# Performance work log

Hardware: AMD Instinct MI355X
Metric: run time of the kernel (lower is better)

## Reference

```python
import jax, jax.numpy as jnp
import numpy as np

B, T, E, H, V = 64, 512, 512, 512, 50000

def setup_inputs() -> dict:
    key = jax.random.key(0)
    ks = jax.random.split(key, 8)
    x = jax.random.randint(ks[0], (B, T), 0, V)
    h0 = jax.random.normal(ks[1], (B, H), jnp.float32) * 0.1
    c0 = jax.random.normal(ks[2], (B, H), jnp.float32) * 0.1
    emb = jax.random.normal(ks[3], (V, E), jnp.float32) * 0.02
    emb = emb.at[0].set(0.0)  # padding_idx=0
    s_i = 1.0 / np.sqrt(H)
    W_ih = jax.random.uniform(ks[4], (4 * H, E), jnp.float32, -s_i, s_i)
    W_hh = jax.random.uniform(ks[5], (4 * H, H), jnp.float32, -s_i, s_i)
    b_ih = jax.random.uniform(ks[6], (4 * H,), jnp.float32, -s_i, s_i)
    b_hh = jax.random.uniform(ks[7], (4 * H,), jnp.float32, -s_i, s_i)
    return {"x": x, "h0": h0, "c0": c0, "emb": emb,
            "W_ih": W_ih, "W_hh": W_hh, "b_ih": b_ih, "b_hh": b_hh}

def reference(x, h0, c0, emb, W_ih, W_hh, b_ih, b_hh):
    # embedding lookup (option 'a'): [B, T, E]
    xs = emb[x]
    # precompute input-to-gate projections for all timesteps: [B, T, 4H]
    pre = jnp.einsum('bte,ge->btg', xs, W_ih) + b_ih + b_hh
    pre_t = jnp.swapaxes(pre, 0, 1)  # [T, B, 4H]

    def step(carry, p_t):
        h, c = carry
        gates = p_t + h @ W_hh.T  # [B, 4H]
        i, f, g, o = jnp.split(gates, 4, axis=-1)
        i = jax.nn.sigmoid(i)
        f = jax.nn.sigmoid(f)
        g = jnp.tanh(g)
        o = jax.nn.sigmoid(o)
        c_new = f * c + i * g
        h_new = o * jnp.tanh(c_new)
        return (h_new, c_new), h_new

    _, hs = jax.lax.scan(step, (h0, c0), pre_t)  # hs: [T, B, H]
    # original stacks per-batch lists of per-timestep hidden states -> [B, T, H]
    return jnp.swapaxes(hs, 0, 1)
```

## Files before the change

kernel.cpp:

```cpp
#include <hip/hip_runtime.h>
#include <stdint.h>

typedef __attribute__((ext_vector_type(8))) short short8;
typedef __attribute__((ext_vector_type(4))) float f4;
typedef __attribute__((ext_vector_type(4))) uint32_t u32x4;

#define B_ 64
#define T_ 512
#define E_ 512
#define H_ 512
#define GH 2048

static __device__ __forceinline__ uint16_t f2bf(float f) {
  uint32_t u = __builtin_bit_cast(uint32_t, f);
  uint32_t r = (u + 0x7FFFu + ((u >> 16) & 1u)) >> 16;
  return (uint16_t)r;
}
static __device__ __forceinline__ float bf2f(uint16_t b) {
  return __builtin_bit_cast(float, (uint32_t)b << 16);
}
static __device__ __forceinline__ float sigmoidf_(float x) {
  return 1.0f / (1.0f + __expf(-x));
}
static __device__ __forceinline__ float tanhf_(float x) {
  float e = __expf(-2.0f * fabsf(x));
  float t = (1.0f - e) / (1.0f + e);
  return __builtin_copysignf(t, x);
}

static __device__ __forceinline__ int ld_flag_cc(const int* p) {
  int v;
  asm volatile("global_load_dword %0, %1, off sc0 sc1\n\ts_waitcnt vmcnt(0)"
               : "=v"(v) : "v"(p) : "memory");
  return v;
}
static __device__ __forceinline__ void ld_x4_cc(u32x4* d, const void* p) {
  asm volatile("global_load_dwordx4 %0, %1, off sc0 sc1" : "=v"(*d) : "v"(p));
}
static __device__ __forceinline__ void st_u16_cc(uint16_t* p, uint32_t v) {
  asm volatile("global_store_short %0, %1, off sc0 sc1" :: "v"(p), "v"(v) : "memory");
}
static __device__ __forceinline__ void st_flag_cc(int* p, int v) {
  asm volatile("global_store_dword %0, %1, off sc0 sc1" :: "v"(p), "v"(v) : "memory");
}

__global__ void k_prep(const float* __restrict__ Whh, uint16_t* __restrict__ Whi_g,
                       uint16_t* __restrict__ Wlo_g) {
  int i = blockIdx.x * 256 + threadIdx.x;
  float w = Whh[i];
  uint16_t hi = f2bf(w);
  Whi_g[i] = hi;
  Wlo_g[i] = f2bf(w - bf2f(hi));
}

__global__ void k_init(const float* __restrict__ h0, uint16_t* __restrict__ hHi0,
                       uint16_t* __restrict__ hLo0, int* __restrict__ flags) {
  int i = blockIdx.x * 256 + threadIdx.x;
  if (i < B_ * H_) {
    float v = h0[i];
    uint16_t hi = f2bf(v);
    hHi0[i] = hi;
    hLo0[i] = f2bf(v - bf2f(hi));
  }
  if (i < 128) flags[i] = 0;
}

__launch_bounds__(256)
__global__ void k_pre(const int* __restrict__ x, const float* __restrict__ emb,
                      const float* __restrict__ Wih, const float* __restrict__ bih,
                      const float* __restrict__ bhh, float* __restrict__ pre2, int t0) {
  __shared__ uint16_t As[128 * 64];
  __shared__ uint16_t Bs[128 * 64];
  const int tid = threadIdx.x;
  const int tm = blockIdx.x >> 4;
  const int tn = blockIdx.x & 15;
  const int wid = tid >> 6, lane = tid & 63;
  const int wr = wid >> 1, wc = wid & 1;

  const int arow = tid >> 1;
  const int half = tid & 1;
  const int m = tm * 128 + arow;
  const int bb = m & 63;
  const int tt = t0 + (m >> 6);
  const int xid = x[bb * T_ + tt];
  const float* asrc = emb + (size_t)xid * E_ + half * 32;
  const float* bsrc = Wih + (size_t)(tn * 128 + arow) * E_ + half * 32;

  f4 acc[4][4];
#pragma unroll
  for (int a = 0; a < 4; ++a)
#pragma unroll
    for (int b = 0; b < 4; ++b) acc[a][b] = (f4){0.f, 0.f, 0.f, 0.f};

  for (int kk = 0; kk < 8; ++kk) {
    __syncthreads();
#pragma unroll
    for (int gi = 0; gi < 4; ++gi) {
      f4 a0 = *(const f4*)(asrc + kk * 64 + gi * 8);
      f4 a1 = *(const f4*)(asrc + kk * 64 + gi * 8 + 4);
      f4 b0 = *(const f4*)(bsrc + kk * 64 + gi * 8);
      f4 b1 = *(const f4*)(bsrc + kk * 64 + gi * 8 + 4);
      short8 va, vb;
#pragma unroll
      for (int j = 0; j < 4; ++j) {
        va[j] = (short)f2bf(a0[j]); va[4 + j] = (short)f2bf(a1[j]);
        vb[j] = (short)f2bf(b0[j]); vb[4 + j] = (short)f2bf(b1[j]);
      }
      int kq = half * 4 + gi;
      *(short8*)(As + arow * 64 + (kq ^ (arow & 7)) * 8) = va;
      *(short8*)(Bs + arow * 64 + (kq ^ (arow & 7)) * 8) = vb;
    }
    __syncthreads();
#pragma unroll
    for (int ks = 0; ks < 2; ++ks) {
      short8 af[4], bfr[4];
#pragma unroll
      for (int mi = 0; mi < 4; ++mi) {
        int row = wr * 64 + mi * 16 + (lane & 15);
        int kq = ks * 4 + (lane >> 4);
        af[mi] = *(const short8*)(As + row * 64 + (kq ^ (row & 7)) * 8);
      }
#pragma unroll
      for (int ni = 0; ni < 4; ++ni) {
        int row = wc * 64 + ni * 16 + (lane & 15);
        int kq = ks * 4 + (lane >> 4);
        bfr[ni] = *(const short8*)(Bs + row * 64 + (kq ^ (row & 7)) * 8);
      }
#pragma unroll
      for (int mi = 0; mi < 4; ++mi)
#pragma unroll
        for (int ni = 0; ni < 4; ++ni)
          acc[mi][ni] = __builtin_amdgcn_mfma_f32_16x16x32_bf16(af[mi], bfr[ni], acc[mi][ni], 0, 0, 0);
    }
  }
#pragma unroll
  for (int ni = 0; ni < 4; ++ni) {
    int n = tn * 128 + wc * 64 + ni * 16 + (lane & 15);
    float bias = bih[n] + bhh[n];
    int q = n >> 9, u = n & 511;
    int ug = u >> 4, uloc = u & 15;
    int gl = q * 16 + uloc;
#pragma unroll
    for (int mi = 0; mi < 4; ++mi) {
      int mrow = tm * 128 + wr * 64 + mi * 16 + (lane >> 4) * 4;
      int trel = mrow >> 6;
      int bbr = mrow & 63;
      f4 vst;
#pragma unroll
      for (int j = 0; j < 4; ++j) vst[j] = acc[mi][ni][j] + bias;
      float* dst = pre2 + (((size_t)trel * 32 + ug) * 4 + (bbr >> 4)) * 1024 + gl * 16 + (bbr & 15);
      *(f4*)dst = vst;
    }
  }
}

__launch_bounds__(256)
__global__ void k_lstm(const float* __restrict__ pre2, const uint16_t* __restrict__ Whi_g,
                       const uint16_t* __restrict__ Wlo_g, const float* __restrict__ c0,
                       float* __restrict__ out, uint16_t* __restrict__ hHi0,
                       uint16_t* __restrict__ hHi1, uint16_t* __restrict__ hLo0,
                       uint16_t* __restrict__ hLo1, float* __restrict__ c_state,
                       int* __restrict__ flags, int t0, int TB) {
  extern __shared__ char smem[];
  uint16_t* WhiL = (uint16_t*)smem;
  uint16_t* WloL = (uint16_t*)(smem + 65536);
  uint16_t* Hh   = (uint16_t*)(smem + 131072);
  uint16_t* Hl   = (uint16_t*)(smem + 147456);

  const int tid = threadIdx.x;
  const int bg = blockIdx.x & 3;
  const int ug = blockIdx.x >> 2;
  const int wv = tid >> 6, lane = tid & 63;
  const int wi = lane & 15, hi4 = lane >> 4;
  const int q = wi & 3, v = wi >> 2;
  const int u = ug * 16 + wv * 4 + v;
  const int gl = q * 16 + wv * 4 + v;

  for (int it = 0; it < 16; ++it) {
    int gg = it * 256 + tid;
    int r = gg >> 6, kq = gg & 63;
    int grow = (r & 3) * 512 + ug * 16 + (r >> 4) * 4 + ((r >> 2) & 3);
    short8 whi = *(const short8*)(Whi_g + (size_t)grow * 512 + kq * 8);
    short8 wlo = *(const short8*)(Wlo_g + (size_t)grow * 512 + kq * 8);
    int kqs = (kq & ~7) | ((kq & 7) ^ (r & 7));
    *(short8*)(WhiL + r * 512 + kqs * 8) = whi;
    *(short8*)(WloL + r * 512 + kqs * 8) = wlo;
  }

  f4 c_reg;
  {
    const float* csrc = (t0 == 0) ? c0 : c_state;
    const int brow = bg * 16 + hi4 * 4;
#pragma unroll
    for (int j = 0; j < 4; ++j) c_reg[j] = csrc[(size_t)(brow + j) * H_ + u];
  }
  int* myflag = flags + bg * 32 + ug;
  __syncthreads();

  for (int s = t0 + 1; s <= t0 + TB; ++s) {
    const uint16_t* hsHi = (((s - 1) & 1) ? hHi1 : hHi0) + (size_t)bg * 16 * 512;
    const uint16_t* hsLo = (((s - 1) & 1) ? hLo1 : hLo0) + (size_t)bg * 16 * 512;
    uint16_t* hdHi = ((s & 1) ? hHi1 : hHi0) + (size_t)bg * 16 * 512;
    uint16_t* hdLo = ((s & 1) ? hLo1 : hLo0) + (size_t)bg * 16 * 512;

    f4 accA, accB, accC;
    {
      const float* pblk = pre2 + (((size_t)(s - 1 - t0) * 32 + ug) * 4 + bg) * 1024;
      accA = *(const f4*)(pblk + gl * 16 + hi4 * 4);
      accB = (f4){0.f, 0.f, 0.f, 0.f};
      accC = accB;
    }

    if (lane < 32) {
      const int* fp = flags + bg * 32 + lane;
      const int target = s - 1;
      int guard = 0;
      while (ld_flag_cc(fp) < target) {
        __builtin_amdgcn_s_sleep(1);
        if (++guard > (1 << 20)) break;
      }
    }

    u32x4 dh[4], dl[4];
#pragma unroll
    for (int jj = 0; jj < 4; ++jj) ld_x4_cc(&dh[jj], hsHi + (size_t)(jj * 256 + tid) * 8);
#pragma unroll
    for (int jj = 0; jj < 4; ++jj) ld_x4_cc(&dl[jj], hsLo + (size_t)(jj * 256 + tid) * 8);
    asm volatile("s_waitcnt vmcnt(0)" ::: "memory");
    __builtin_amdgcn_sched_barrier(0);
#pragma unroll
    for (int jj = 0; jj < 4; ++jj) { asm volatile("" : "+v"(dh[jj])); asm volatile("" : "+v"(dl[jj])); }
#pragma unroll
    for (int jj = 0; jj < 4; ++jj) {
      int gidx = jj * 256 + tid;
      int row = gidx >> 6, kq = gidx & 63;
      int kqs = (kq & ~7) | ((kq & 7) ^ (row & 7));
      *(u32x4*)(Hh + row * 512 + kqs * 8) = dh[jj];
      *(u32x4*)(Hl + row * 512 + kqs * 8) = dl[jj];
    }
    __syncthreads();

    const int br = wv * 16 + wi;
#pragma unroll 4
    for (int ks = 0; ks < 16; ++ks) {
      int kq = ks * 4 + hi4;
      int kqsA = (kq & ~7) | ((kq & 7) ^ (wi & 7));
      int kqsB = (kq & ~7) | ((kq & 7) ^ (br & 7));
      short8 ah = *(const short8*)(Hh + wi * 512 + kqsA * 8);
      short8 al = *(const short8*)(Hl + wi * 512 + kqsA * 8);
      short8 bh = *(const short8*)(WhiL + br * 512 + kqsB * 8);
      short8 bl = *(const short8*)(WloL + br * 512 + kqsB * 8);
      accA = __builtin_amdgcn_mfma_f32_16x16x32_bf16(ah, bh, accA, 0, 0, 0);
      accB = __builtin_amdgcn_mfma_f32_16x16x32_bf16(al, bh, accB, 0, 0, 0);
      accC = __builtin_amdgcn_mfma_f32_16x16x32_bf16(ah, bl, accC, 0, 0, 0);
    }

    const bool qb0 = (q & 1) != 0, qb1 = (q & 2) != 0;
    const int b = bg * 16 + hi4 * 4 + q;
    f4 a0;
#pragma unroll
    for (int j = 0; j < 4; ++j) a0[j] = accA[j] + accB[j] + accC[j];
    f4 x1, s1a, s1b, x2a, x2b;
#pragma unroll
    for (int j = 0; j < 4; ++j) x1[j] = __shfl_xor(a0[j], 1);
#pragma unroll
    for (int j = 0; j < 4; ++j) {
      s1a[j] = qb0 ? x1[j] : a0[j];
      s1b[j] = qb0 ? a0[j] : x1[j];
    }
#pragma unroll
    for (int j = 0; j < 4; ++j) {
      x2a[j] = __shfl_xor(s1a[j], 2);
      x2b[j] = __shfl_xor(s1b[j], 2);
    }
    f4 cn, hn;
#pragma unroll
    for (int j = 0; j < 4; ++j) {
      float gi = qb1 ? x2a[j] : s1a[j];
      float gg = qb1 ? s1a[j] : x2a[j];
      float gf = qb1 ? x2b[j] : s1b[j];
      float go = qb1 ? s1b[j] : x2b[j];
      float iv = sigmoidf_(gi);
      float fv = sigmoidf_(gf);
      float gv = tanhf_(gg);
      float ov = sigmoidf_(go);
      float c2 = fv * c_reg[j] + iv * gv;
      cn[j] = c2;
      hn[j] = ov * tanhf_(c2);
    }
    c_reg = cn;
    float s01 = qb0 ? hn[1] : hn[0];
    float s23 = qb0 ? hn[3] : hn[2];
    float hq = qb1 ? s23 : s01;

    uint16_t hhi = f2bf(hq);
    uint16_t hlo = f2bf(hq - bf2f(hhi));
    const int rowloc = hi4 * 4 + q;
    st_u16_cc(hdHi + (size_t)rowloc * 512 + u, (uint32_t)hhi);
    st_u16_cc(hdLo + (size_t)rowloc * 512 + u, (uint32_t)hlo);
    asm volatile("s_waitcnt vmcnt(0)" ::: "memory");
    __syncthreads();
    if (tid == 0) st_flag_cc(myflag, s);
    __builtin_nontemporal_store(hq, &out[(size_t)b * (T_ * H_) + (size_t)(s - 1) * H_ + u]);
  }

  {
    const bool qb0 = (q & 1) != 0, qb1 = (q & 2) != 0;
    const int b = bg * 16 + hi4 * 4 + q;
    float c01 = qb0 ? c_reg[1] : c_reg[0];
    float c23 = qb0 ? c_reg[3] : c_reg[2];
    c_state[(size_t)b * H_ + u] = qb1 ? c23 : c01;
  }
}

extern "C" void kernel_launch(void* const* d_in, const int* in_sizes, int n_in,
                              void* d_out, int out_size, void* d_ws, size_t ws_size,
                              hipStream_t stream) {
  (void)in_sizes; (void)n_in; (void)out_size;
  const int* x = (const int*)d_in[0];
  const float* h0 = (const float*)d_in[1];
  const float* c0 = (const float*)d_in[2];
  const float* emb = (const float*)d_in[3];
  const float* Wih = (const float*)d_in[4];
  const float* Whh = (const float*)d_in[5];
  const float* bih = (const float*)d_in[6];
  const float* bhh = (const float*)d_in[7];
  float* out = (float*)d_out;
  char* ws = (char*)d_ws;

  int* flags = (int*)ws;
  float* c_state = (float*)(ws + 4096);
  uint16_t* hHi0 = (uint16_t*)(ws + 135168);
  uint16_t* hHi1 = (uint16_t*)(ws + 135168 + 65536);
  uint16_t* hLo0 = (uint16_t*)(ws + 135168 + 2 * 65536);
  uint16_t* hLo1 = (uint16_t*)(ws + 135168 + 3 * 65536);
  uint16_t* Whi_g = (uint16_t*)(ws + 397312);
  uint16_t* Wlo_g = (uint16_t*)(ws + 2494464);
  float* pre2 = (float*)(ws + 4591616);

  int TB = 512;
  while (TB > 2 && (size_t)4591616 + (size_t)TB * 524288 > ws_size) TB >>= 1;

  (void)hipFuncSetAttribute(reinterpret_cast<const void*>(k_lstm),
                            hipFuncAttributeMaxDynamicSharedMemorySize, 163840);

  k_prep<<<dim3(4096), dim3(256), 0, stream>>>(Whh, Whi_g, Wlo_g);
  k_init<<<dim3(128), dim3(256), 0, stream>>>(h0, hHi0, hLo0, flags);
  for (int t0 = 0; t0 < 512; t0 += TB) {
    k_pre<<<dim3((TB * 64 / 128) * 16), dim3(256), 0, stream>>>(x, emb, Wih, bih, bhh, pre2, t0);
    k_lstm<<<dim3(128), dim3(256), 163840, stream>>>(pre2, Whi_g, Wlo_g, c0, out, hHi0, hHi1,
                                                     hLo0, hLo1, c_state, flags, t0, TB);
  }
}
```

Baseline: 2.484 ms.

## Pack hi/lo hidden state into one word and use per-wave flags

The bf16 hi and lo halves of each hidden value are now packed into a single 32-bit word, so the exchange between recurrent steps needs one store and one load stream instead of two. Readiness flags become per-wave (four per block), so each wave polls only the producers of its own 128-column slice and signals right after its own store, which removes the block-wide barrier before the flag store. A barrier after the MFMA loop protects the shared hidden-state buffers, and the sleep in the spin loop is dropped. The trade-off is more flag traffic and polling, plus unpacking work when writing shared memory.

```diff
diff --git a/kernel.cpp b/kernel.cpp
--- a/kernel.cpp
+++ b/kernel.cpp
@@ -2,6 +2,7 @@
 #include <stdint.h>
 
 typedef __attribute__((ext_vector_type(8))) short short8;
+typedef __attribute__((ext_vector_type(4))) short short4_;
 typedef __attribute__((ext_vector_type(4))) float f4;
 typedef __attribute__((ext_vector_type(4))) uint32_t u32x4;
 
@@ -37,8 +38,8 @@
 static __device__ __forceinline__ void ld_x4_cc(u32x4* d, const void* p) {
   asm volatile("global_load_dwordx4 %0, %1, off sc0 sc1" : "=v"(*d) : "v"(p));
 }
-static __device__ __forceinline__ void st_u16_cc(uint16_t* p, uint32_t v) {
-  asm volatile("global_store_short %0, %1, off sc0 sc1" :: "v"(p), "v"(v) : "memory");
+static __device__ __forceinline__ void st_u32_cc(uint32_t* p, uint32_t v) {
+  asm volatile("global_store_dword %0, %1, off sc0 sc1" :: "v"(p), "v"(v) : "memory");
 }
 static __device__ __forceinline__ void st_flag_cc(int* p, int v) {
   asm volatile("global_store_dword %0, %1, off sc0 sc1" :: "v"(p), "v"(v) : "memory");
@@ -53,16 +54,16 @@
   Wlo_g[i] = f2bf(w - bf2f(hi));
 }
 
-__global__ void k_init(const float* __restrict__ h0, uint16_t* __restrict__ hHi0,
-                       uint16_t* __restrict__ hLo0, int* __restrict__ flags) {
+__global__ void k_init(const float* __restrict__ h0, uint32_t* __restrict__ hP0,
+                       int* __restrict__ flags) {
   int i = blockIdx.x * 256 + threadIdx.x;
   if (i < B_ * H_) {
     float v = h0[i];
     uint16_t hi = f2bf(v);
-    hHi0[i] = hi;
-    hLo0[i] = f2bf(v - bf2f(hi));
-  }
-  if (i < 128) flags[i] = 0;
+    uint16_t lo = f2bf(v - bf2f(hi));
+    hP0[i] = (uint32_t)hi | ((uint32_t)lo << 16);
+  }
+  if (i < 512) flags[i] = 0;
 }
 
 __launch_bounds__(256)
@@ -157,9 +158,8 @@
 __launch_bounds__(256)
 __global__ void k_lstm(const float* __restrict__ pre2, const uint16_t* __restrict__ Whi_g,
                        const uint16_t* __restrict__ Wlo_g, const float* __restrict__ c0,
-                       float* __restrict__ out, uint16_t* __restrict__ hHi0,
-                       uint16_t* __restrict__ hHi1, uint16_t* __restrict__ hLo0,
-                       uint16_t* __restrict__ hLo1, float* __restrict__ c_state,
+                       float* __restrict__ out, uint32_t* __restrict__ hP0,
+                       uint32_t* __restrict__ hP1, float* __restrict__ c_state,
                        int* __restrict__ flags, int t0, int TB) {
   extern __shared__ char smem[];
   uint16_t* WhiL = (uint16_t*)smem;
@@ -194,14 +194,13 @@
 #pragma unroll
     for (int j = 0; j < 4; ++j) c_reg[j] = csrc[(size_t)(brow + j) * H_ + u];
   }
-  int* myflag = flags + bg * 32 + ug;
+  int* fl = flags + bg * 128;
+  int* myflag = fl + ug * 4 + wv;
   __syncthreads();
 
   for (int s = t0 + 1; s <= t0 + TB; ++s) {
-    const uint16_t* hsHi = (((s - 1) & 1) ? hHi1 : hHi0) + (size_t)bg * 16 * 512;
-    const uint16_t* hsLo = (((s - 1) & 1) ? hLo1 : hLo0) + (size_t)bg * 16 * 512;
-    uint16_t* hdHi = ((s & 1) ? hHi1 : hHi0) + (size_t)bg * 16 * 512;
-    uint16_t* hdLo = ((s & 1) ? hLo1 : hLo0) + (size_t)bg * 16 * 512;
+    const uint32_t* hsrc = (((s - 1) & 1) ? hP1 : hP0) + (size_t)bg * 16 * 512;
+    uint32_t* hdst = (s & 1) ? hP1 : hP0;
 
     f4 accA, accB, accC;
     {
@@ -212,31 +211,41 @@
     }
 
     if (lane < 32) {
-      const int* fp = flags + bg * 32 + lane;
+      const int* fp = fl + wv * 32 + lane;
       const int target = s - 1;
       int guard = 0;
       while (ld_flag_cc(fp) < target) {
-        __builtin_amdgcn_s_sleep(1);
-        if (++guard > (1 << 20)) break;
-      }
-    }
-
-    u32x4 dh[4], dl[4];
-#pragma unroll
-    for (int jj = 0; jj < 4; ++jj) ld_x4_cc(&dh[jj], hsHi + (size_t)(jj * 256 + tid) * 8);
-#pragma unroll
-    for (int jj = 0; jj < 4; ++jj) ld_x4_cc(&dl[jj], hsLo + (size_t)(jj * 256 + tid) * 8);
+        if (++guard > (1 << 16)) break;
+      }
+    }
+
+    u32x4 d[8];
+#pragma unroll
+    for (int jj = 0; jj < 8; ++jj) {
+      int local = jj * 64 + lane;
+      int row = local >> 5;
+      int u0v = wv * 128 + (local & 31) * 4;
+      ld_x4_cc(&d[jj], hsrc + (size_t)row * 512 + u0v);
+    }
     asm volatile("s_waitcnt vmcnt(0)" ::: "memory");
     __builtin_amdgcn_sched_barrier(0);
 #pragma unroll
-    for (int jj = 0; jj < 4; ++jj) { asm volatile("" : "+v"(dh[jj])); asm volatile("" : "+v"(dl[jj])); }
-#pragma unroll
-    for (int jj = 0; jj < 4; ++jj) {
-      int gidx = jj * 256 + tid;
-      int row = gidx >> 6, kq = gidx & 63;
+    for (int jj = 0; jj < 8; ++jj) asm volatile("" : "+v"(d[jj]));
+#pragma unroll
+    for (int jj = 0; jj < 8; ++jj) {
+      int local = jj * 64 + lane;
+      int row = local >> 5;
+      int u0v = wv * 128 + (local & 31) * 4;
+      int kq = u0v >> 3, half = (u0v >> 2) & 1;
       int kqs = (kq & ~7) | ((kq & 7) ^ (row & 7));
-      *(u32x4*)(Hh + row * 512 + kqs * 8) = dh[jj];
-      *(u32x4*)(Hl + row * 512 + kqs * 8) = dl[jj];
+      short4_ hh, hl;
+#pragma unroll
+      for (int i = 0; i < 4; ++i) {
+        hh[i] = (short)(d[jj][i] & 0xFFFFu);
+        hl[i] = (short)(d[jj][i] >> 16);
+      }
+      *(short4_*)(Hh + row * 512 + kqs * 8 + half * 4) = hh;
+      *(short4_*)(Hl + row * 512 + kqs * 8 + half * 4) = hl;
     }
     __syncthreads();
 
@@ -254,9 +263,11 @@
       accB = __builtin_amdgcn_mfma_f32_16x16x32_bf16(al, bh, accB, 0, 0, 0);
       accC = __builtin_amdgcn_mfma_f32_16x16x32_bf16(ah, bl, accC, 0, 0, 0);
     }
+    __syncthreads();
 
     const bool qb0 = (q & 1) != 0, qb1 = (q & 2) != 0;
-    const int b = bg * 16 + hi4 * 4 + q;
+    const int rowloc = hi4 * 4 + q;
+    const int b = bg * 16 + rowloc;
     f4 a0;
 #pragma unroll
     for (int j = 0; j < 4; ++j) a0[j] = accA[j] + accB[j] + accC[j];
@@ -295,12 +306,9 @@
 
     uint16_t hhi = f2bf(hq);
     uint16_t hlo = f2bf(hq - bf2f(hhi));
-    const int rowloc = hi4 * 4 + q;
-    st_u16_cc(hdHi + (size_t)rowloc * 512 + u, (uint32_t)hhi);
-    st_u16_cc(hdLo + (size_t)rowloc * 512 + u, (uint32_t)hlo);
+    st_u32_cc(hdst + (size_t)b * 512 + u, (uint32_t)hhi | ((uint32_t)hlo << 16));
     asm volatile("s_waitcnt vmcnt(0)" ::: "memory");
-    __syncthreads();
-    if (tid == 0) st_flag_cc(myflag, s);
+    if (lane == 0) st_flag_cc(myflag, s);
     __builtin_nontemporal_store(hq, &out[(size_t)b * (T_ * H_) + (size_t)(s - 1) * H_ + u]);
   }
 
@@ -330,10 +338,8 @@
 
   int* flags = (int*)ws;
   float* c_state = (float*)(ws + 4096);
-  uint16_t* hHi0 = (uint16_t*)(ws + 135168);
-  uint16_t* hHi1 = (uint16_t*)(ws + 135168 + 65536);
-  uint16_t* hLo0 = (uint16_t*)(ws + 135168 + 2 * 65536);
-  uint16_t* hLo1 = (uint16_t*)(ws + 135168 + 3 * 65536);
+  uint32_t* hP0 = (uint32_t*)(ws + 135168);
+  uint32_t* hP1 = (uint32_t*)(ws + 266240);
   uint16_t* Whi_g = (uint16_t*)(ws + 397312);
   uint16_t* Wlo_g = (uint16_t*)(ws + 2494464);
   float* pre2 = (float*)(ws + 4591616);
@@ -345,10 +351,10 @@
                             hipFuncAttributeMaxDynamicSharedMemorySize, 163840);
 
   k_prep<<<dim3(4096), dim3(256), 0, stream>>>(Whh, Whi_g, Wlo_g);
-  k_init<<<dim3(128), dim3(256), 0, stream>>>(h0, hHi0, hLo0, flags);
+  k_init<<<dim3(128), dim3(256), 0, stream>>>(h0, hP0, flags);
   for (int t0 = 0; t0 < 512; t0 += TB) {
     k_pre<<<dim3((TB * 64 / 128) * 16), dim3(256), 0, stream>>>(x, emb, Wih, bih, bhh, pre2, t0);
-    k_lstm<<<dim3(128), dim3(256), 163840, stream>>>(pre2, Whi_g, Wlo_g, c0, out, hHi0, hHi1,
-                                                     hLo0, hLo1, c_state, flags, t0, TB);
-  }
-}
+    k_lstm<<<dim3(128), dim3(256), 163840, stream>>>(pre2, Whi_g, Wlo_g, c0, out, hP0, hP1,
+                                                     c_state, flags, t0, TB);
+  }
+}
```

Measured after the change: 3.318 ms. 1.34x slower.
